# Kernel tuning notes

Measured on AMD Instinct MI355X. Metric: run time of the kernel, lower is better.

The kernel has to match this reference:

```python
import jax, jax.numpy as jnp
import numpy as np

B, N, E, K = 4, 8192, 1024, 2048  # batch, points, emb_dims, pool nodes (N//4)
KNN = 20


def _conv(w, x):  # 1x1 Conv1d, no bias: w [O,C], x [B,C,N]
    return jnp.einsum('oc,bcn->bon', w, x)


def _bn(x, s, b):  # eval-mode BN folded to per-channel scale/bias, x [B,C,N]
    return x * s[None, :, None] + b[None, :, None]


def _sqdist(a, b):  # a [B,3,N], b [B,3,M] -> [B,N,M] squared distances
    return ((a * a).sum(1)[:, :, None] + (b * b).sum(1)[:, None, :]
            - 2.0 * jnp.einsum('bcn,bcm->bnm', a, b))


def _bgather(f, idx):  # f [B,C,N], idx [B,...] -> [B,C,...]
    return jax.vmap(lambda ff, ii: ff[:, ii])(f, idx)


def _pool(xyz, feat, pw, pb, k):
    Bq, C, _ = feat.shape
    proj = _conv(pw, feat) + pb[None, :, None]          # [B,8C,N]
    vec = proj.max(-1).reshape(Bq, C, 8)                # [B,C,8]
    scores = jax.nn.sigmoid(jnp.einsum('bcn,bce->bne', feat, vec))  # [B,N,8]
    v, i = jax.lax.top_k(scores.transpose(0, 2, 1), k // 8)         # [B,8,k//8]
    values = v.transpose(0, 2, 1).reshape(Bq, -1)       # [B,k] (torch reshape order)
    idx = i.transpose(0, 2, 1).reshape(Bq, -1)
    node_static = _bgather(xyz, idx)                    # [B,3,k]
    node_feature = _bgather(feat, idx) * values[:, None, :]
    node = node_static * values[:, None, :]
    return node, node_feature, node_static


def _aggregate(xyz, node, feat, k):
    d = _sqdist(xyz, node)                               # [B,N,M]
    _, idx = jax.lax.top_k(-d.transpose(0, 2, 1), k)     # [B,M,k] nearest inputs per node
    grouped = _bgather(feat, idx)                        # [B,C,M,k]
    return grouped.max(-1)                               # [B,C,M]


def _unpool(node_xyz, unknown_xyz, feat):
    d = _sqdist(unknown_xyz, node_xyz)                   # [B,N,M]
    negd, idx = jax.lax.top_k(-d, 3)                     # 3-NN along M
    w = jax.nn.softmax(-negd, axis=-1)                   # softmax over sq-dists (faithful)
    grouped = _bgather(feat, idx)                        # [B,C,N,3]
    return (w[:, None, :, :] * grouped).sum(-1)


def _forward(x, conv1_w, bn1_s, bn1_b, conv2_w, bn2_s, bn2_b,
             conv2m_w, bn2m_s, bn2m_b, pool_w, pool_b,
             conv3_w, bn3_s, bn3_b, conv4_w, bn4_s, bn4_b,
             conv5_w, bn5_s, bn5_b, conv6_w, bn6c_s, bn6c_b,
             conv7_w, bn7c_s, bn7c_b, conv8_w, bn8_s, bn8_b,
             conv9_w, bn9_s, bn9_b, conv10_w,
             lin1_w, bn6h_s, bn6h_b, lin2_w, lin2_b, bn7h_s, bn7h_b,
             lin3_w, lin3_b):
    relu = jax.nn.relu
    xyz = x
    x1 = relu(_bn(_conv(conv1_w, x), bn1_s, bn1_b))      # [B,64,N]
    x2 = relu(_bn(_conv(conv2_w, x1), bn2_s, bn2_b))     # [B,64,N]
    xt1_ = jnp.concatenate([x1, x2], 1)                  # [B,128,N]
    xt1 = relu(_bn(_conv(conv2m_w, xt1_), bn2m_s, bn2m_b))  # [B,E,N]
    node1, nf1, node1_static = _pool(xyz, xt1_, pool_w, pool_b, K)
    agg = _aggregate(xyz, node1, xt1_, KNN)              # [B,128,K]
    h = jnp.concatenate([nf1, agg], 1)                   # [B,256,K]
    x3 = relu(_bn(_conv(conv3_w, h), bn3_s, bn3_b))
    x4 = relu(_bn(_conv(conv4_w, x3), bn4_s, bn4_b))
    xt2 = relu(_bn(_conv(conv5_w, jnp.concatenate([x3, x4], 1)), bn5_s, bn5_b))
    vector = jnp.concatenate([xt1.max(-1), xt2.max(-1)], 1)  # [B,2E]
    c = relu((vector @ lin1_w.T) * bn6h_s + bn6h_b)
    c = relu((c @ lin2_w.T + lin2_b) * bn7h_s + bn7h_b)
    logits_cls = c @ lin3_w.T + lin3_b                   # [B,15]
    vrep = jnp.broadcast_to(vector[:, :, None], (vector.shape[0], vector.shape[1], x4.shape[-1]))
    s = relu(_bn(_conv(conv6_w, jnp.concatenate([vrep, x4], 1)), bn6c_s, bn6c_b))
    s = relu(_bn(_conv(conv7_w, jnp.concatenate([s, x3], 1)), bn7c_s, bn7c_b))
    s = _unpool(node1, xyz, s)                           # [B,128,N]
    s = relu(_bn(_conv(conv8_w, jnp.concatenate([s, x2], 1)), bn8_s, bn8_b))
    s = relu(_bn(_conv(conv9_w, jnp.concatenate([s, x1], 1)), bn9_s, bn9_b))
    logits_seg = _conv(conv10_w, s)                      # [B,2,N]
    return (logits_cls, logits_seg, node1, node1_static)


def setup_inputs() -> dict:
    key = jax.random.key(0)
    keys = iter(jax.random.split(key, 80))
    def w(shape, scale=0.05):
        return jax.random.normal(next(keys), shape, jnp.float32) * scale
    inp = {'x': jax.random.normal(next(keys), (B, 3, N), jnp.float32)}
    conv_shapes = {'conv1_w': (64, 3), 'conv2_w': (64, 64), 'conv2m_w': (E, 128),
                   'conv3_w': (256, 256), 'conv4_w': (256, 256), 'conv5_w': (E, 512),
                   'conv6_w': (128, 2 * E + 256), 'conv7_w': (128, 384),
                   'conv8_w': (128, 192), 'conv9_w': (128, 192), 'conv10_w': (2, 128)}
    for n, s in conv_shapes.items():
        inp[n] = w(s)
    for n, c in [('bn1', 64), ('bn2', 64), ('bn2m', E), ('bn3', 256), ('bn4', 256),
                 ('bn5', E), ('bn6c', 128), ('bn7c', 128), ('bn8', 128), ('bn9', 128),
                 ('bn6h', 512), ('bn7h', 256)]:
        inp[n + '_s'] = 1.0 + w((c,))
        inp[n + '_b'] = w((c,))
    inp['pool_w'] = w((E, 128)); inp['pool_b'] = w((E,))
    inp['lin1_w'] = w((512, 2 * E))
    inp['lin2_w'] = w((256, 512)); inp['lin2_b'] = w((256,))
    inp['lin3_w'] = w((15, 256)); inp['lin3_b'] = w((15,))
    return inp


def reference(x, conv1_w, bn1_s, bn1_b, conv2_w, bn2_s, bn2_b,
              conv2m_w, bn2m_s, bn2m_b, pool_w, pool_b,
              conv3_w, bn3_s, bn3_b, conv4_w, bn4_s, bn4_b,
              conv5_w, bn5_s, bn5_b, conv6_w, bn6c_s, bn6c_b,
              conv7_w, bn7c_s, bn7c_b, conv8_w, bn8_s, bn8_b,
              conv9_w, bn9_s, bn9_b, conv10_w,
              lin1_w, bn6h_s, bn6h_b, lin2_w, lin2_b, bn7h_s, bn7h_b,
              lin3_w, lin3_b):
    return _forward(x, conv1_w, bn1_s, bn1_b, conv2_w, bn2_s, bn2_b,
                    conv2m_w, bn2m_s, bn2m_b, pool_w, pool_b,
                    conv3_w, bn3_s, bn3_b, conv4_w, bn4_s, bn4_b,
                    conv5_w, bn5_s, bn5_b, conv6_w, bn6c_s, bn6c_b,
                    conv7_w, bn7c_s, bn7c_b, conv8_w, bn8_s, bn8_b,
                    conv9_w, bn9_s, bn9_b, conv10_w,
                    lin1_w, bn6h_s, bn6h_b, lin2_w, lin2_b, bn7h_s, bn7h_b,
                    lin3_w, lin3_b)
```

## Files before the change

kernel.cpp:

```cpp
#include <hip/hip_runtime.h>
#include <math.h>

typedef unsigned short u16;
typedef short bf8 __attribute__((ext_vector_type(8)));
typedef float f4 __attribute__((ext_vector_type(4)));

#define NPTS 8192
#define MNODE 2048

#define WS_XT1  0L
#define WS_A    4194304L
#define WS_B    8388608L
#define WS_C    12582912L
#define WS_D    14680064L
#define WS_TOPV 18874368L
#define WS_TOPI 18882560L
#define WS_NODE 18890752L
#define WS_MAXP 18915328L
#define WS_VEC  18919424L
#define WS_C1   18927616L
#define WS_C2   18929664L
#define WS_B6   18930688L
#define WS_K20  18931200L
#define WS_K3I  19095040L
#define WS_K3W  19193344L

__device__ __forceinline__ u16 bf16rne(float f) {
    unsigned u = __float_as_uint(f);
    unsigned r = u + 0x7FFFu + ((u >> 16) & 1u);
    return (u16)(r >> 16);
}

__global__ __launch_bounds__(256) void k_conv1(const float* __restrict__ x,
                                               const float* __restrict__ W,
                                               const float* __restrict__ sc,
                                               const float* __restrict__ bi,
                                               float* __restrict__ out) {
    int t = blockIdx.x * 256 + threadIdx.x;
    int n = t & 8191, o = (t >> 13) & 63, b = t >> 19;
    const float* xb = x + (long)b * 3 * NPTS;
    float a = W[o * 3 + 0] * xb[n] + W[o * 3 + 1] * xb[NPTS + n] + W[o * 3 + 2] * xb[2 * NPTS + n];
    a = fmaxf(a * sc[o] + bi[o], 0.f);
    out[((long)b * 128 + o) * NPTS + n] = a;
}


__global__ __launch_bounds__(256) void k_packall(
        const float* __restrict__ c2mw, const float* __restrict__ c3w,
        const float* __restrict__ c4w,  const float* __restrict__ c5w,
        const float* __restrict__ c6w,  const float* __restrict__ c7w,
        const float* __restrict__ c8w,  const float* __restrict__ c9w,
        u16* __restrict__ d2m, u16* __restrict__ d3, u16* __restrict__ d4,
        u16* __restrict__ d5,  u16* __restrict__ d6, u16* __restrict__ d7,
        u16* __restrict__ d8,  u16* __restrict__ d9) {
    int t = blockIdx.x * 256 + threadIdx.x;
    const float* W; u16* dst; int C, wp, base;
    if (t < 131072)      { W = c2mw;       dst = d2m; C = 128; wp = 128;  base = 0; }
    else if (t < 196608) { W = c3w;        dst = d3;  C = 256; wp = 256;  base = 131072; }
    else if (t < 262144) { W = c4w;        dst = d4;  C = 256; wp = 256;  base = 196608; }
    else if (t < 786432) { W = c5w;        dst = d5;  C = 512; wp = 512;  base = 262144; }
    else if (t < 819200) { W = c6w + 2048; dst = d6;  C = 256; wp = 2304; base = 786432; }
    else if (t < 868352) { W = c7w;        dst = d7;  C = 384; wp = 384;  base = 819200; }
    else if (t < 892928) { W = c8w;        dst = d8;  C = 192; wp = 192;  base = 868352; }
    else if (t < 917504) { W = c9w;        dst = d9;  C = 192; wp = 192;  base = 892928; }
    else return;
    int u = t - base;
    int o = u / C, p = u - o * C;
    int blk = p >> 5, pj = p & 31;
    int g = pj >> 3, j = pj & 7;
    int k = (blk << 5) + g * 4 + (j & 3) + 16 * (j >> 2);
    dst[u] = bf16rne(W[(long)o * wp + k]);
}

__global__ __launch_bounds__(256) void k_packT2(const float* __restrict__ in, long ibs,
                                                int C, int Nn, u16* __restrict__ out,
                                                int opitch, int coff) {
    __shared__ float tile[32][33];
    int b = blockIdx.z;
    int k0 = blockIdx.y * 32, n0 = blockIdx.x * 32;
    int tx = threadIdx.x & 31, ty = threadIdx.x >> 5;
    for (int r = 0; r < 32; r += 8)
        tile[ty + r][tx] = in[(long)b * ibs + (long)(k0 + ty + r) * Nn + n0 + tx];
    __syncthreads();
    for (int r = 0; r < 32; r += 8) {
        int n = n0 + ty + r;
        int p = tx;
        int g = p >> 3, j = p & 7;
        int kin = g * 4 + (j & 3) + 16 * (j >> 2);
        out[((long)b * Nn + n) * opitch + coff + k0 + p] = bf16rne(tile[kin][ty + r]);
    }
}

__global__ __launch_bounds__(256) void k_packT2d(const float* __restrict__ in1, long ibs1, int C1,
                                                 const float* __restrict__ in2, long ibs2, int C2,
                                                 int Nn, u16* __restrict__ out, int opitch) {
    __shared__ float tile[32][33];
    int b = blockIdx.z;
    int y1 = C1 >> 5;
    const float* in; int k0, coff;
    if ((int)blockIdx.y < y1) { in = in1 + (long)b * ibs1; k0 = blockIdx.y * 32; coff = 0; }
    else { in = in2 + (long)b * ibs2; k0 = ((int)blockIdx.y - y1) * 32; coff = C1; }
    int n0 = blockIdx.x * 32;
    int tx = threadIdx.x & 31, ty = threadIdx.x >> 5;
    for (int r = 0; r < 32; r += 8)
        tile[ty + r][tx] = in[(long)(k0 + ty + r) * Nn + n0 + tx];
    __syncthreads();
    for (int r = 0; r < 32; r += 8) {
        int n = n0 + ty + r;
        int p = tx, g = p >> 3, j = p & 7;
        int kin = g * 4 + (j & 3) + 16 * (j >> 2);
        out[((long)b * Nn + n) * opitch + coff + k0 + p] = bf16rne(tile[kin][ty + r]);
    }
}

__global__ __launch_bounds__(256) void k_cvmx_bf(const u16* __restrict__ in,
                                                 const u16* __restrict__ wpk, int C,
                                                 const float* __restrict__ sc,
                                                 const float* __restrict__ bi, int do_relu,
                                                 float* __restrict__ pmax, int O, int Nn) {
    __shared__ float red[4][16][17];
    int b = blockIdx.z, nc = blockIdx.x;
    int lane = threadIdx.x & 63, w = threadIdx.x >> 6;
    int o0 = (blockIdx.y * 4 + w) * 16;
    const u16* wp = wpk + (long)(o0 + (lane & 15)) * C + ((lane >> 4) << 3);
    const u16* ip = in + ((long)b * Nn + nc * 256 + (lane & 15)) * C + ((lane >> 4) << 3);
    long nstride = 16L * C;
    f4 acc[16];
#pragma unroll
    for (int t = 0; t < 16; ++t) acc[t] = (f4)(0.f);
    for (int kk = 0; kk < C; kk += 32) {
        bf8 a = *(const bf8*)(wp + kk);
#pragma unroll
        for (int t = 0; t < 16; ++t) {
            bf8 bb = *(const bf8*)(ip + t * nstride + kk);
            acc[t] = __builtin_amdgcn_mfma_f32_16x16x32_bf16(a, bb, acc[t], 0, 0, 0);
        }
    }
#pragma unroll
    for (int j = 0; j < 4; ++j) {
        int ol = (lane >> 4) * 4 + j;
        int o = o0 + ol;
        float scv = sc ? sc[o] : 1.f;
        float biv = bi ? bi[o] : 0.f;
        float mm = -3.0e38f;
#pragma unroll
        for (int t = 0; t < 16; ++t) {
            float v = acc[t][j] * scv + biv;
            if (do_relu) v = fmaxf(v, 0.f);
            mm = fmaxf(mm, v);
        }
        red[w][ol][lane & 15] = mm;
    }
    __syncthreads();
    if (threadIdx.x < 64) {
        int ww = threadIdx.x >> 4, oo = threadIdx.x & 15;
        float mm = red[ww][oo][0];
#pragma unroll
        for (int i = 1; i < 16; ++i) mm = fmaxf(mm, red[ww][oo][i]);
        int og = (blockIdx.y * 4 + ww) * 16 + oo;
        pmax[((long)nc * 4 + b) * O + og] = mm;
    }
}

__global__ __launch_bounds__(256) void k_conv_bf(const u16* __restrict__ in,
                                                 int C,
                                                 const u16* __restrict__ wpk,
                                                 const float* __restrict__ sc,
                                                 const float* __restrict__ bi, int do_relu,
                                                 float* __restrict__ out, long obs, int Nn) {
    int b = blockIdx.z, nc = blockIdx.x;
    int lane = threadIdx.x & 63, w = threadIdx.x >> 6;
    int o0 = (blockIdx.y * 4 + w) * 16;
    const u16* wp = wpk + (long)(o0 + (lane & 15)) * C + ((lane >> 4) << 3);
    const u16* ip = in + ((long)b * Nn + nc * 256 + (lane & 15)) * C + ((lane >> 4) << 3);
    long nstride = 16L * C;
    f4 acc[16];
#pragma unroll
    for (int t = 0; t < 16; ++t) acc[t] = (f4)(0.f);
    for (int kk = 0; kk < C; kk += 32) {
        bf8 a = *(const bf8*)(wp + kk);
#pragma unroll
        for (int t = 0; t < 16; ++t) {
            bf8 bb = *(const bf8*)(ip + t * nstride + kk);
            acc[t] = __builtin_amdgcn_mfma_f32_16x16x32_bf16(a, bb, acc[t], 0, 0, 0);
        }
    }
#pragma unroll
    for (int j = 0; j < 4; ++j) {
        int o = o0 + (lane >> 4) * 4 + j;
        float scv = sc ? sc[o] : 1.f;
        float biv = bi ? bi[o] : 0.f;
        float* op = out + (long)b * obs + (long)o * Nn + nc * 256 + (lane & 15);
#pragma unroll
        for (int t = 0; t < 16; ++t) {
            float v = acc[t][j] * scv + biv;
            if (do_relu) v = fmaxf(v, 0.f);
            op[t * 16] = v;
        }
    }
}

__global__ __launch_bounds__(256) void k_conv_bf2(
        const u16* __restrict__ in1, int p1, int C1,
        const u16* __restrict__ in2, int p2, int C2,
        const u16* __restrict__ wpk,
        const float* __restrict__ extra,
        const float* __restrict__ sc, const float* __restrict__ bi, int do_relu,
        float* __restrict__ out, long obs, int O, int Nn) {
    int b = blockIdx.z, nc = blockIdx.x;
    int lane = threadIdx.x & 63, w = threadIdx.x >> 6;
    int o0 = (blockIdx.y * 4 + w) * 16;
    int Ct = C1 + C2;
    const u16* wp = wpk + (long)(o0 + (lane & 15)) * Ct + ((lane >> 4) << 3);
    f4 acc[16];
#pragma unroll
    for (int t = 0; t < 16; ++t) acc[t] = (f4)(0.f);
    {
        const u16* ip1 = in1 + ((long)b * Nn + nc * 256 + (lane & 15)) * p1 + ((lane >> 4) << 3);
        long ns1 = 16L * p1;
        for (int kk = 0; kk < C1; kk += 32) {
            bf8 a = *(const bf8*)(wp + kk);
#pragma unroll
            for (int t = 0; t < 16; ++t) {
                bf8 bb = *(const bf8*)(ip1 + t * ns1 + kk);
                acc[t] = __builtin_amdgcn_mfma_f32_16x16x32_bf16(a, bb, acc[t], 0, 0, 0);
            }
        }
    }
    if (in2) {
        const u16* ip2 = in2 + ((long)b * Nn + nc * 256 + (lane & 15)) * p2 + ((lane >> 4) << 3);
        long ns2 = 16L * p2;
        for (int kk = 0; kk < C2; kk += 32) {
            bf8 a = *(const bf8*)(wp + C1 + kk);
#pragma unroll
            for (int t = 0; t < 16; ++t) {
                bf8 bb = *(const bf8*)(ip2 + t * ns2 + kk);
                acc[t] = __builtin_amdgcn_mfma_f32_16x16x32_bf16(a, bb, acc[t], 0, 0, 0);
            }
        }
    }
#pragma unroll
    for (int j = 0; j < 4; ++j) {
        int o = o0 + (lane >> 4) * 4 + j;
        float e = extra ? extra[(long)b * O + o] : 0.f;
        float scv = sc ? sc[o] : 1.f;
        float biv = bi ? bi[o] : 0.f;
        float* op = out + (long)b * obs + (long)o * Nn + nc * 256 + (lane & 15);
#pragma unroll
        for (int t = 0; t < 16; ++t) {
            float v = (acc[t][j] + e) * scv + biv;
            if (do_relu) v = fmaxf(v, 0.f);
            op[t * 16] = v;
        }
    }
}

#define CMAX_FMA16()                                                        \
    {                                                                       \
        const float4* wp4 = reinterpret_cast<const float4*>(Wl + c16);      \
        _Pragma("unroll")                                                   \
        for (int g = 0; g < 4; ++g) {                                       \
            float4 w = wp4[g];                                              \
            acc[4 * g + 0].x = fmaf(w.x, v.x, acc[4 * g + 0].x);            \
            acc[4 * g + 0].y = fmaf(w.x, v.y, acc[4 * g + 0].y);            \
            acc[4 * g + 0].z = fmaf(w.x, v.z, acc[4 * g + 0].z);            \
            acc[4 * g + 0].w = fmaf(w.x, v.w, acc[4 * g + 0].w);            \
            acc[4 * g + 1].x = fmaf(w.y, v.x, acc[4 * g + 1].x);            \
            acc[4 * g + 1].y = fmaf(w.y, v.y, acc[4 * g + 1].y);            \
            acc[4 * g + 1].z = fmaf(w.y, v.z, acc[4 * g + 1].z);            \
            acc[4 * g + 1].w = fmaf(w.y, v.w, acc[4 * g + 1].w);            \
            acc[4 * g + 2].x = fmaf(w.z, v.x, acc[4 * g + 2].x);            \
            acc[4 * g + 2].y = fmaf(w.z, v.y, acc[4 * g + 2].y);            \
            acc[4 * g + 2].z = fmaf(w.z, v.z, acc[4 * g + 2].z);            \
            acc[4 * g + 2].w = fmaf(w.z, v.w, acc[4 * g + 2].w);            \
            acc[4 * g + 3].x = fmaf(w.w, v.x, acc[4 * g + 3].x);            \
            acc[4 * g + 3].y = fmaf(w.w, v.y, acc[4 * g + 3].y);            \
            acc[4 * g + 3].z = fmaf(w.w, v.z, acc[4 * g + 3].z);            \
            acc[4 * g + 3].w = fmaf(w.w, v.w, acc[4 * g + 3].w);            \
        }                                                                   \
    }

__global__ __launch_bounds__(256) void k_convmax(
        const float* __restrict__ in, int C, long ibs,
        const float* __restrict__ W1, const float* __restrict__ cb1,
        const float* __restrict__ sc1, const float* __restrict__ bi1, int relu1,
        float* __restrict__ pmax1,
        const float* __restrict__ W2, const float* __restrict__ cb2,
        const float* __restrict__ sc2, const float* __restrict__ bi2, int relu2,
        float* __restrict__ pmax2,
        int wpitch, int O, int Nn) {
    extern __shared__ float sm_[];
    float* Wl = sm_;
    float* red = sm_;
    int b = blockIdx.z;
    int ns = blockIdx.x;
    int oblocks = O >> 4;
    int setid = (int)blockIdx.y / oblocks;
    int og0 = ((int)blockIdx.y - setid * oblocks) * 16;
    const float* W  = setid ? W2 : W1;
    const float* cb = setid ? cb2 : cb1;
    const float* sc = setid ? sc2 : sc1;
    const float* bi = setid ? bi2 : bi1;
    int do_relu     = setid ? relu2 : relu1;
    float* pmax     = setid ? pmax2 : pmax1;
    for (int t = threadIdx.x; t < 16 * C; t += 256) {
        int c = t >> 4, o = t & 15;
        Wl[t] = W[(long)(og0 + o) * wpitch + c];
    }
    __syncthreads();
    int n0 = ns * 1024 + threadIdx.x * 4;
    float4 acc[16];
#pragma unroll
    for (int o = 0; o < 16; ++o) acc[o] = make_float4(0.f, 0.f, 0.f, 0.f);
    const float* p = in + (long)b * ibs + n0;
    float4 v = *reinterpret_cast<const float4*>(p);
    for (int c = 0; c < C - 1; ++c) {
        float4 vn = *reinterpret_cast<const float4*>(p + (long)(c + 1) * Nn);
        int c16 = c * 16;
        CMAX_FMA16();
        v = vn;
    }
    {
        int c16 = (C - 1) * 16;
        CMAX_FMA16();
    }
    float h2[16];
#pragma unroll
    for (int o = 0; o < 16; ++o) {
        float cbv = cb ? cb[og0 + o] : 0.f;
        float scv = sc ? sc[og0 + o] : 1.f;
        float biv = bi ? bi[og0 + o] : 0.f;
        float4 a = acc[o];
        float vx = (a.x + cbv) * scv + biv;
        float vy = (a.y + cbv) * scv + biv;
        float vz = (a.z + cbv) * scv + biv;
        float vw = (a.w + cbv) * scv + biv;
        if (do_relu) {
            vx = fmaxf(vx, 0.f); vy = fmaxf(vy, 0.f);
            vz = fmaxf(vz, 0.f); vw = fmaxf(vw, 0.f);
        }
        h2[o] = fmaxf(fmaxf(vx, vy), fmaxf(vz, vw));
    }
    __syncthreads();
#pragma unroll
    for (int o = 0; o < 16; ++o) red[o * 257 + threadIdx.x] = h2[o];
    __syncthreads();
    for (int ls = 7; ls >= 0; --ls) {
        int s = 1 << ls;
        for (int w = threadIdx.x; w < 16 * s; w += 256) {
            int o = w >> ls, i = w & (s - 1);
            float* r = red + o * 257;
            r[i] = fmaxf(r[i], r[i + s]);
        }
        __syncthreads();
    }
    if (threadIdx.x < 16)
        pmax[((long)ns * 4 + b) * O + og0 + threadIdx.x] = red[threadIdx.x * 257];
}

__global__ __launch_bounds__(256) void k_maxred2(const float* __restrict__ pA, int nsA, int OA,
                                                 float* __restrict__ outA, long obsA,
                                                 const float* __restrict__ pB, int nsB, int OB,
                                                 float* __restrict__ outB, long obsB,
                                                 int blocksA) {
    const float* pm; int ns, O; float* out; long obs; int bid = blockIdx.x;
    if (bid < blocksA) { pm = pA; ns = nsA; O = OA; out = outA; obs = obsA; }
    else { pm = pB; ns = nsB; O = OB; out = outB; obs = obsB; bid -= blocksA; }
    int t = bid * 256 + threadIdx.x;
    if (t >= 4 * O) return;
    int o = t % O, b = t / O;
    float m = -3.0e38f;
    for (int s = 0; s < ns; ++s) m = fmaxf(m, pm[((long)s * 4 + b) * O + o]);
    out[(long)b * obs + o] = m;
}

__global__ __launch_bounds__(256) void k_maxred(const float* __restrict__ pmax, int nsplit,
                                                int O, float* __restrict__ out, long obs) {
    int t = blockIdx.x * 256 + threadIdx.x;
    if (t >= 4 * O) return;
    int o = t % O, b = t / O;
    float m = -3.0e38f;
    for (int s = 0; s < nsplit; ++s) m = fmaxf(m, pmax[((long)s * 4 + b) * O + o]);
    out[(long)b * obs + o] = m;
}

#define CONV_FMA8()                                                         \
    {                                                                       \
        const float4* wp4 = reinterpret_cast<const float4*>(Wl + c8);       \
        _Pragma("unroll")                                                   \
        for (int g = 0; g < 2; ++g) {                                       \
            float4 w = wp4[g];                                              \
            acc[4 * g + 0].x = fmaf(w.x, v.x, acc[4 * g + 0].x);            \
            acc[4 * g + 0].y = fmaf(w.x, v.y, acc[4 * g + 0].y);            \
            acc[4 * g + 0].z = fmaf(w.x, v.z, acc[4 * g + 0].z);            \
            acc[4 * g + 0].w = fmaf(w.x, v.w, acc[4 * g + 0].w);            \
            acc[4 * g + 1].x = fmaf(w.y, v.x, acc[4 * g + 1].x);            \
            acc[4 * g + 1].y = fmaf(w.y, v.y, acc[4 * g + 1].y);            \
            acc[4 * g + 1].z = fmaf(w.y, v.z, acc[4 * g + 1].z);            \
            acc[4 * g + 1].w = fmaf(w.y, v.w, acc[4 * g + 1].w);            \
            acc[4 * g + 2].x = fmaf(w.z, v.x, acc[4 * g + 2].x);            \
            acc[4 * g + 2].y = fmaf(w.z, v.y, acc[4 * g + 2].y);            \
            acc[4 * g + 2].z = fmaf(w.z, v.z, acc[4 * g + 2].z);            \
            acc[4 * g + 2].w = fmaf(w.z, v.w, acc[4 * g + 2].w);            \
            acc[4 * g + 3].x = fmaf(w.w, v.x, acc[4 * g + 3].x);            \
            acc[4 * g + 3].y = fmaf(w.w, v.y, acc[4 * g + 3].y);            \
            acc[4 * g + 3].z = fmaf(w.w, v.z, acc[4 * g + 3].z);            \
            acc[4 * g + 3].w = fmaf(w.w, v.w, acc[4 * g + 3].w);            \
        }                                                                   \
    }

__global__ __launch_bounds__(256) void k_conv(const float* __restrict__ in1, int C1, long ibs1,
                                              const float* __restrict__ in2, int C2, long ibs2,
                                              const float* __restrict__ W, int wpitch,
                                              const float* __restrict__ extra,
                                              const float* __restrict__ sc,
                                              const float* __restrict__ bi, int do_relu,
                                              float* __restrict__ out, long obs, int O, int Nn) {
    __shared__ float Wl[384 * 8];
    int b = blockIdx.z;
    int og0 = blockIdx.y * 8;
    int on = O - og0; if (on > 8) on = 8;
    int Ct = C1 + C2;
    for (int t = threadIdx.x; t < Ct * 8; t += 256) {
        int c = t >> 3, o = t & 7;
        Wl[t] = (o < on) ? W[(long)(og0 + o) * wpitch + c] : 0.f;
    }
    __syncthreads();
    int n0 = blockIdx.x * 1024 + threadIdx.x * 4;
    float4 acc[8];
#pragma unroll
    for (int o = 0; o < 8; ++o) acc[o] = make_float4(0.f, 0.f, 0.f, 0.f);
    const float* p1 = in1 + (long)b * ibs1 + n0;
    {
        float4 v = *reinterpret_cast<const float4*>(p1);
        for (int c = 0; c < C1 - 1; ++c) {
            float4 vn = *reinterpret_cast<const float4*>(p1 + (long)(c + 1) * Nn);
            int c8 = c * 8;
            CONV_FMA8();
            v = vn;
        }
        int c8 = (C1 - 1) * 8;
        CONV_FMA8();
    }
    if (in2) {
        const float* p2 = in2 + (long)b * ibs2 + n0;
        float4 v = *reinterpret_cast<const float4*>(p2);
        for (int c = 0; c < C2 - 1; ++c) {
            float4 vn = *reinterpret_cast<const float4*>(p2 + (long)(c + 1) * Nn);
            int c8 = (C1 + c) * 8;
            CONV_FMA8();
            v = vn;
        }
        int c8 = (Ct - 1) * 8;
        CONV_FMA8();
    }
#pragma unroll
    for (int o = 0; o < 8; ++o) {
        if (o < on) {
            float e = extra ? extra[(long)b * O + og0 + o] : 0.f;
            float s = sc ? sc[og0 + o] : 1.f;
            float bv = bi ? bi[og0 + o] : 0.f;
            float4 a = acc[o];
            a.x = (a.x + e) * s + bv;
            a.y = (a.y + e) * s + bv;
            a.z = (a.z + e) * s + bv;
            a.w = (a.w + e) * s + bv;
            if (do_relu) {
                a.x = fmaxf(a.x, 0.f); a.y = fmaxf(a.y, 0.f);
                a.z = fmaxf(a.z, 0.f); a.w = fmaxf(a.w, 0.f);
            }
            *reinterpret_cast<float4*>(out + (long)b * obs + (long)(og0 + o) * Nn + n0) = a;
        }
    }
}

__global__ __launch_bounds__(256) void k_scores(const float* __restrict__ feat,
                                                const float* __restrict__ maxp,
                                                float* __restrict__ scores) {
    __shared__ float vl[1024];
    int b = blockIdx.z;
    for (int t = threadIdx.x; t < 1024; t += 256) vl[t] = maxp[b * 1024 + t];
    __syncthreads();
    int n = blockIdx.x * 256 + threadIdx.x;
    float acc[8];
#pragma unroll
    for (int e = 0; e < 8; ++e) acc[e] = 0.f;
    const float* p = feat + (long)b * 128 * NPTS + n;
    float v = p[0];
    for (int c = 0; c < 127; ++c) {
        float vn = p[(long)(c + 1) * NPTS];
#pragma unroll
        for (int e = 0; e < 8; ++e) acc[e] = fmaf(vl[c * 8 + e], v, acc[e]);
        v = vn;
    }
#pragma unroll
    for (int e = 0; e < 8; ++e) acc[e] = fmaf(vl[127 * 8 + e], v, acc[e]);
#pragma unroll
    for (int e = 0; e < 8; ++e)
        scores[((long)b * 8 + e) * NPTS + n] = 1.f / (1.f + expf(-acc[e]));
}

__global__ __launch_bounds__(256) void k_sorta(const float* __restrict__ scores,
                                               unsigned int* __restrict__ kout,
                                               unsigned short* __restrict__ iout) {
    __shared__ unsigned int kv[1024];
    __shared__ unsigned short ki[1024];
    int ch = blockIdx.x & 7;
    const float* sp = scores + (long)(blockIdx.x >> 3) * NPTS + ch * 1024;
    for (int t = threadIdx.x; t < 1024; t += 256) {
        kv[t] = __float_as_uint(sp[t]) ^ 0xFFFFFFFFu;
        ki[t] = (unsigned short)(ch * 1024 + t);
    }
    __syncthreads();
    for (int k = 2; k <= 1024; k <<= 1) {
        for (int j = k >> 1; j > 0; j >>= 1) {
            for (int t = threadIdx.x; t < 1024; t += 256) {
                int ixj = t ^ j;
                if (ixj > t) {
                    unsigned int va = kv[t], vb = kv[ixj];
                    unsigned short ia = ki[t], ib = ki[ixj];
                    bool up = ((t & k) == 0);
                    bool gt = (va > vb) || (va == vb && ia > ib);
                    if (gt == up) { kv[t] = vb; kv[ixj] = va; ki[t] = ib; ki[ixj] = ia; }
                }
            }
            __syncthreads();
        }
    }
    if (threadIdx.x < 256) {
        kout[blockIdx.x * 256 + threadIdx.x] = kv[threadIdx.x];
        iout[blockIdx.x * 256 + threadIdx.x] = ki[threadIdx.x];
    }
}

__global__ __launch_bounds__(512) void k_sortb(const unsigned int* __restrict__ kin,
                                               const unsigned short* __restrict__ iin,
                                               float* __restrict__ topv,
                                               int* __restrict__ topi) {
    __shared__ unsigned int kv[2048];
    __shared__ unsigned short ki[2048];
    int be = blockIdx.x, b = be >> 3, e = be & 7;
    for (int t = threadIdx.x; t < 2048; t += 512) {
        kv[t] = kin[be * 2048 + t];
        ki[t] = iin[be * 2048 + t];
    }
    __syncthreads();
    for (int k = 2; k <= 2048; k <<= 1) {
        for (int j = k >> 1; j > 0; j >>= 1) {
            for (int t = threadIdx.x; t < 2048; t += 512) {
                int ixj = t ^ j;
                if (ixj > t) {
                    unsigned int va = kv[t], vb = kv[ixj];
                    unsigned short ia = ki[t], ib = ki[ixj];
                    bool up = ((t & k) == 0);
                    bool gt = (va > vb) || (va == vb && ia > ib);
                    if (gt == up) { kv[t] = vb; kv[ixj] = va; ki[t] = ib; ki[ixj] = ia; }
                }
            }
            __syncthreads();
        }
    }
    for (int r = threadIdx.x; r < 256; r += 512) {
        int j = r * 8 + e;
        topv[b * 2048 + j] = __uint_as_float(kv[r] ^ 0xFFFFFFFFu);
        topi[b * 2048 + j] = (int)ki[r];
    }
}

__global__ __launch_bounds__(256) void k_gather(const float* __restrict__ feat,
                                                const float* __restrict__ xyz,
                                                const float* __restrict__ topv,
                                                const int* __restrict__ topi,
                                                float* __restrict__ h,
                                                float* __restrict__ node_ws,
                                                float* __restrict__ out_node,
                                                float* __restrict__ out_nstat) {
    int bid = blockIdx.x;
    if (bid < 4096) {
        int t = bid * 256 + threadIdx.x;
        int j = t & 2047, c = (t >> 11) & 127, b = t >> 18;
        int i = topi[b * 2048 + j];
        float v = topv[b * 2048 + j];
        h[((long)b * 256 + c) * MNODE + j] = feat[((long)b * 128 + c) * NPTS + i] * v;
    } else {
        int t = (bid - 4096) * 256 + threadIdx.x;
        int j = t & 2047, b = t >> 11;
        int i = topi[b * 2048 + j];
        float v = topv[b * 2048 + j];
#pragma unroll
        for (int k = 0; k < 3; ++k) {
            float sx = xyz[((long)b * 3 + k) * NPTS + i];
            float nd = sx * v;
            out_nstat[((long)b * 3 + k) * MNODE + j] = sx;
            out_node[((long)b * 3 + k) * MNODE + j] = nd;
            node_ws[((long)b * 3 + k) * MNODE + j] = nd;
        }
    }
}

__device__ __forceinline__ unsigned int fsortbits(float f) {
    unsigned int u = __float_as_uint(f);
    return u ^ ((unsigned int)((int)u >> 31) | 0x80000000u);
}

__global__ __launch_bounds__(256) void k_knn20(const float* __restrict__ xyz,
                                               const float* __restrict__ node,
                                               int* __restrict__ k20) {
    __shared__ unsigned int s1[256];
    __shared__ int s2[256];
    __shared__ int lcnt;
    int m = blockIdx.x & 2047, b = blockIdx.x >> 11;
    int t = threadIdx.x;
    float nx = node[((long)b * 3 + 0) * MNODE + m];
    float ny = node[((long)b * 3 + 1) * MNODE + m];
    float nz = node[((long)b * 3 + 2) * MNODE + m];
    float sm = nx * nx + ny * ny + nz * nz;
    const float* xb = xyz + (long)b * 3 * NPTS;
    unsigned int kmin = 0xFFFFFFFFu;
    for (int i = 0; i < 32; ++i) {
        int n = i * 256 + t;
        float px = xb[n], py = xb[NPTS + n], pz = xb[2 * NPTS + n];
        float d = (px * px + py * py + pz * pz) + sm - 2.f * (px * nx + py * ny + pz * nz);
        unsigned int key = fsortbits(d);
        kmin = key < kmin ? key : kmin;
    }
    s1[t] = kmin;
    if (t == 0) lcnt = 0;
    __syncthreads();
    for (int k = 2; k <= 256; k <<= 1) {
        for (int j = k >> 1; j > 0; j >>= 1) {
            int ixj = t ^ j;
            if (ixj > t) {
                unsigned int va = s1[t], vb = s1[ixj];
                bool up = ((t & k) == 0);
                if ((va > vb) == up) { s1[t] = vb; s1[ixj] = va; }
            }
            __syncthreads();
        }
    }
    unsigned int keyT = s1[19];
    __syncthreads();
    for (int i = 0; i < 32; ++i) {
        int n = i * 256 + t;
        float px = xb[n], py = xb[NPTS + n], pz = xb[2 * NPTS + n];
        float d = (px * px + py * py + pz * pz) + sm - 2.f * (px * nx + py * ny + pz * nz);
        unsigned int key = fsortbits(d);
        if (key <= keyT) {
            int p = atomicAdd(&lcnt, 1);
            if (p < 128) { s1[p] = key; s2[p] = n; }
        }
    }
    __syncthreads();
    int cnt = lcnt;
    if (cnt <= 128) {
        if (t >= cnt && t < 128) { s1[t] = 0xFFFFFFFFu; s2[t] = 0x7FFFFFFF; }
        __syncthreads();
        for (int k = 2; k <= 128; k <<= 1) {
            for (int j = k >> 1; j > 0; j >>= 1) {
                if (t < 128) {
                    int ixj = t ^ j;
                    if (ixj > t) {
                        unsigned int va = s1[t], vb = s1[ixj];
                        int ia = s2[t], ib = s2[ixj];
                        bool up = ((t & k) == 0);
                        bool gt = (va > vb) || (va == vb && ia > ib);
                        if (gt == up) { s1[t] = vb; s1[ixj] = va; s2[t] = ib; s2[ixj] = ia; }
                    }
                }
                __syncthreads();
            }
        }
        if (t < 20) k20[((long)b * 2048 + m) * 20 + t] = s2[t];
    } else {
        unsigned int lastk = 0u; int lasti = -1;
        for (int r = 0; r < 20; ++r) {
            unsigned int bk = 0xFFFFFFFFu; int bi = 0x7FFFFFFF;
            for (int i = 0; i < 32; ++i) {
                int n = i * 256 + t;
                float px = xb[n], py = xb[NPTS + n], pz = xb[2 * NPTS + n];
                float d = (px * px + py * py + pz * pz) + sm - 2.f * (px * nx + py * ny + pz * nz);
                unsigned int key = fsortbits(d);
                bool gtlast = (key > lastk) || (key == lastk && n > lasti);
                bool ltbest = (key < bk) || (key == bk && n < bi);
                if (gtlast && ltbest) { bk = key; bi = n; }
            }
            s1[t] = bk; s2[t] = bi;
            __syncthreads();
            for (int s = 128; s > 0; s >>= 1) {
                if (t < s) {
                    unsigned int vo = s1[t + s]; int io = s2[t + s];
                    unsigned int vm = s1[t]; int im = s2[t];
                    if (vo < vm || (vo == vm && io < im)) { s1[t] = vo; s2[t] = io; }
                }
                __syncthreads();
            }
            if (t == 0) k20[((long)b * 2048 + m) * 20 + r] = s2[0];
            lastk = s1[0]; lasti = s2[0];
            __syncthreads();
        }
    }
}

__global__ __launch_bounds__(256) void k_agg(const float* __restrict__ feat,
                                             const int* __restrict__ k20,
                                             float* __restrict__ h) {
    int t = blockIdx.x * 256 + threadIdx.x;
    int m = t & 2047, c = (t >> 11) & 127, b = t >> 18;
    const int* ip = k20 + ((long)b * 2048 + m) * 20;
    const float* fb = feat + ((long)b * 128 + c) * NPTS;
    float mx = -3.0e38f;
#pragma unroll
    for (int q = 0; q < 20; ++q) mx = fmaxf(mx, fb[ip[q] & 8191]);
    h[((long)b * 256 + 128 + c) * MNODE + m] = mx;
}

__global__ __launch_bounds__(256) void k_gemv(const float* __restrict__ in, int C,
                                              const float* __restrict__ W, int wpitch,
                                              const float* __restrict__ lb,
                                              const float* __restrict__ sc,
                                              const float* __restrict__ bi, int do_relu,
                                              float* __restrict__ out, int O) {
    __shared__ float red[256];
    int o = blockIdx.x;
    int t = threadIdx.x;
    const float* wp = W + (long)o * wpitch;
    float a0 = 0.f, a1 = 0.f, a2 = 0.f, a3 = 0.f;
    for (int c = t * 4; c < C; c += 1024) {
        float4 w = *reinterpret_cast<const float4*>(wp + c);
        float4 v0 = *reinterpret_cast<const float4*>(in + 0L * C + c);
        float4 v1 = *reinterpret_cast<const float4*>(in + 1L * C + c);
        float4 v2 = *reinterpret_cast<const float4*>(in + 2L * C + c);
        float4 v3 = *reinterpret_cast<const float4*>(in + 3L * C + c);
        a0 += w.x * v0.x + w.y * v0.y + w.z * v0.z + w.w * v0.w;
        a1 += w.x * v1.x + w.y * v1.y + w.z * v1.z + w.w * v1.w;
        a2 += w.x * v2.x + w.y * v2.y + w.z * v2.z + w.w * v2.w;
        a3 += w.x * v3.x + w.y * v3.y + w.z * v3.z + w.w * v3.w;
    }
    float lbv = lb ? lb[o] : 0.f;
    float scv = sc ? sc[o] : 1.f;
    float biv = bi ? bi[o] : 0.f;
#pragma unroll
    for (int b = 0; b < 4; ++b) {
        float a = (b == 0) ? a0 : (b == 1) ? a1 : (b == 2) ? a2 : a3;
        __syncthreads();
        red[t] = a;
        __syncthreads();
        for (int s2 = 128; s2 > 0; s2 >>= 1) {
            if (t < s2) red[t] += red[t + s2];
            __syncthreads();
        }
        if (t == 0) {
            float r = (red[0] + lbv) * scv + biv;
            if (do_relu) r = fmaxf(r, 0.f);
            out[(long)b * O + o] = r;
        }
    }
}

__global__ __launch_bounds__(256) void k_knn3(const float* __restrict__ xyz,
                                              const float* __restrict__ node,
                                              int* __restrict__ k3i, float* __restrict__ k3w) {
    __shared__ float sx[2048], sy[2048], sz[2048], sn[2048];
    __shared__ float md[256][3];
    __shared__ int   mi[256][3];
    int b = blockIdx.x >> 8;
    int pbase = (blockIdx.x & 255) * 32;
    int t = threadIdx.x;
    const float* nb = node + (long)b * 3 * MNODE;
    for (int j = t; j < 2048; j += 256) {
        float qx = nb[j], qy = nb[MNODE + j], qz = nb[2 * MNODE + j];
        sx[j] = qx; sy[j] = qy; sz[j] = qz;
        sn[j] = qx * qx + qy * qy + qz * qz;
    }
    __syncthreads();
    int i = t & 31, q = t >> 5;
    int n = pbase + i;
    float px = xyz[((long)b * 3 + 0) * NPTS + n];
    float py = xyz[((long)b * 3 + 1) * NPTS + n];
    float pz = xyz[((long)b * 3 + 2) * NPTS + n];
    float sp = px * px + py * py + pz * pz;
    float d0 = 3.0e38f, d1 = 3.0e38f, d2 = 3.0e38f;
    int i0 = 0, i1 = 0, i2 = 0;
    int m0 = q * 256;
#pragma unroll 4
    for (int k = 0; k < 256; ++k) {
        int m = m0 + k;
        float d = (sp + sn[m]) - 2.f * (px * sx[m] + py * sy[m] + pz * sz[m]);
        if (d < d2) {
            d2 = d; i2 = m;
            if (d2 < d1) { float td = d1; d1 = d2; d2 = td; int ti = i1; i1 = i2; i2 = ti; }
            if (d1 < d0) { float td = d0; d0 = d1; d1 = td; int ti = i0; i0 = i1; i1 = ti; }
        }
    }
    md[t][0] = d0; md[t][1] = d1; md[t][2] = d2;
    mi[t][0] = i0; mi[t][1] = i1; mi[t][2] = i2;
    __syncthreads();
    if (t < 32) {
        int p0 = 0, p1 = 0, p2 = 0, p3 = 0, p4 = 0, p5 = 0, p6 = 0, p7 = 0;
        float rd[3]; int ri[3];
#pragma unroll
        for (int r = 0; r < 3; ++r) {
            float bestd = 3.0e38f; int besti = 0x7FFFFFFF; int bestq = -1;
#define KNN3_HEAD(QQ, PV)                                                              \
            {                                                                          \
                float dd = md[(QQ) * 32 + t][PV]; int ii = mi[(QQ) * 32 + t][PV];      \
                if (dd < bestd || (dd == bestd && ii < besti)) {                       \
                    bestd = dd; besti = ii; bestq = (QQ);                              \
                }                                                                      \
            }
            KNN3_HEAD(0, p0) KNN3_HEAD(1, p1) KNN3_HEAD(2, p2) KNN3_HEAD(3, p3)
            KNN3_HEAD(4, p4) KNN3_HEAD(5, p5) KNN3_HEAD(6, p6) KNN3_HEAD(7, p7)
#undef KNN3_HEAD
            rd[r] = bestd; ri[r] = besti;
            p0 += (bestq == 0); p1 += (bestq == 1); p2 += (bestq == 2); p3 += (bestq == 3);
            p4 += (bestq == 4); p5 += (bestq == 5); p6 += (bestq == 6); p7 += (bestq == 7);
        }
        float mxd = fmaxf(rd[0], fmaxf(rd[1], rd[2]));
        float e0 = expf(rd[0] - mxd), e1 = expf(rd[1] - mxd), e2 = expf(rd[2] - mxd);
        float inv = 1.f / (e0 + e1 + e2);
        long base = ((long)b * NPTS + pbase + t) * 3;
        k3i[base] = ri[0]; k3i[base + 1] = ri[1]; k3i[base + 2] = ri[2];
        k3w[base] = e0 * inv; k3w[base + 1] = e1 * inv; k3w[base + 2] = e2 * inv;
    }
}

__global__ __launch_bounds__(256) void k_unpool(const float* __restrict__ s7,
                                                const int* __restrict__ k3i,
                                                const float* __restrict__ k3w,
                                                float* __restrict__ sup) {
    int t = blockIdx.x * 256 + threadIdx.x;
    int n = t & 8191, c = (t >> 13) & 127, b = t >> 20;
    long base = ((long)b * NPTS + n) * 3;
    const float* spp = s7 + ((long)b * 128 + c) * MNODE;
    float a = k3w[base] * spp[k3i[base]] + k3w[base + 1] * spp[k3i[base + 1]] +
              k3w[base + 2] * spp[k3i[base + 2]];
    sup[((long)b * 128 + c) * NPTS + n] = a;
}

extern "C" void kernel_launch(void* const* d_in, const int* in_sizes, int n_in,
                              void* d_out, int out_size, void* d_ws, size_t ws_size,
                              hipStream_t stream) {
    const float* x     = (const float*)d_in[0];
    const float* c1w   = (const float*)d_in[1];
    const float* c2w   = (const float*)d_in[2];
    const float* c2mw  = (const float*)d_in[3];
    const float* c3w   = (const float*)d_in[4];
    const float* c4w   = (const float*)d_in[5];
    const float* c5w   = (const float*)d_in[6];
    const float* c6w   = (const float*)d_in[7];
    const float* c7w   = (const float*)d_in[8];
    const float* c8w   = (const float*)d_in[9];
    const float* c9w   = (const float*)d_in[10];
    const float* c10w  = (const float*)d_in[11];
    const float* bn1s  = (const float*)d_in[12]; const float* bn1b  = (const float*)d_in[13];
    const float* bn2s  = (const float*)d_in[14]; const float* bn2b  = (const float*)d_in[15];
    const float* bn2ms = (const float*)d_in[16]; const float* bn2mb = (const float*)d_in[17];
    const float* bn3s  = (const float*)d_in[18]; const float* bn3b  = (const float*)d_in[19];
    const float* bn4s  = (const float*)d_in[20]; const float* bn4b  = (const float*)d_in[21];
    const float* bn5s  = (const float*)d_in[22]; const float* bn5b  = (const float*)d_in[23];
    const float* bn6cs = (const float*)d_in[24]; const float* bn6cb = (const float*)d_in[25];
    const float* bn7cs = (const float*)d_in[26]; const float* bn7cb = (const float*)d_in[27];
    const float* bn8s  = (const float*)d_in[28]; const float* bn8b  = (const float*)d_in[29];
    const float* bn9s  = (const float*)d_in[30]; const float* bn9b  = (const float*)d_in[31];
    const float* bn6hs = (const float*)d_in[32]; const float* bn6hb = (const float*)d_in[33];
    const float* bn7hs = (const float*)d_in[34]; const float* bn7hb = (const float*)d_in[35];
    const float* poolw = (const float*)d_in[36]; const float* poolb = (const float*)d_in[37];
    const float* l1w   = (const float*)d_in[38];
    const float* l2w   = (const float*)d_in[39]; const float* l2b   = (const float*)d_in[40];
    const float* l3w   = (const float*)d_in[41]; const float* l3b   = (const float*)d_in[42];

    float* ws   = (float*)d_ws;
    float* xt1  = ws + WS_XT1;
    float* x34  = ws + WS_A;
    float* s8   = ws + WS_A;
    float* scor = ws + WS_B;
    float* hbuf = ws + WS_C;
    float* s6   = ws + WS_C;
    float* s7   = ws + WS_C + 1048576L;
    float* sup  = ws + WS_D;
    float* s9   = ws + WS_D;
    float* topv = ws + WS_TOPV;
    int*   topi = (int*)(ws + WS_TOPI);
    float* node = ws + WS_NODE;
    float* maxp = ws + WS_MAXP;
    float* vec  = ws + WS_VEC;
    float* c1b  = ws + WS_C1;
    float* c2b_ = ws + WS_C2;
    float* b6   = ws + WS_B6;
    int*   k20  = (int*)(ws + WS_K20);
    float* pmax1 = ws + WS_K20;
    float* pmax2 = ws + WS_K20 + 131072;
    int*   k3i  = (int*)(ws + WS_K3I);
    float* k3w  = ws + WS_K3W;
    unsigned int*   sskeys = (unsigned int*)(ws + WS_A);
    unsigned short* ssidx  = (unsigned short*)(ws + WS_A + 65536);
    u16* xtb   = (u16*)(ws + WS_C);
    u16* c2mwb = (u16*)(ws + WS_D);
    u16* x34b  = (u16*)(ws + WS_B);
    u16* c5wb  = (u16*)(ws + WS_B + 2097152);
    u16* hb    = (u16*)(ws + WS_D);
    u16* x3p   = (u16*)(ws + WS_D + 1048576);
    u16* c3wb  = (u16*)(ws + WS_D + 2097152);
    u16* c4wb  = (u16*)(ws + WS_D + 2129920);
    u16* c6wb  = (u16*)(ws + WS_D + 2162688);
    u16* c7wb  = (u16*)(ws + WS_D + 2179072);
    u16* s6p   = (u16*)(ws + WS_D);
    u16* sp8   = (u16*)(ws + WS_B);
    u16* cc8wb = (u16*)(ws + WS_B + 3145728);
    u16* cc9wb = (u16*)(ws + WS_B + 3158016);
    u16* sp9   = (u16*)(ws + WS_B);

    float* out       = (float*)d_out;
    float* out_cls   = out;
    float* out_seg   = out + 60;
    float* out_node  = out + 60 + 65536;
    float* out_nstat = out_node + 24576;

    k_packall<<<dim3(3584), dim3(256), 0, stream>>>(c2mw, c3w, c4w, c5w, c6w, c7w, c8w, c9w,
                                                    c2mwb, c3wb, c4wb, c5wb, c6wb, c7wb,
                                                    cc8wb, cc9wb);
    k_conv1<<<dim3(8192), dim3(256), 0, stream>>>(x, c1w, bn1s, bn1b, xt1);
    k_conv<<<dim3(8, 8, 4), dim3(256), 0, stream>>>(xt1, 64, 128L * NPTS, nullptr, 0, 0,
                                                    c2w, 64, nullptr, bn2s, bn2b, 1,
                                                    xt1 + 64L * NPTS, 128L * NPTS, 64, NPTS);
    k_packT2<<<dim3(256, 4, 4), dim3(256), 0, stream>>>(xt1, 128L * NPTS, 128, NPTS, xtb, 128, 0);
    k_cvmx_bf<<<dim3(32, 16, 4), dim3(256), 0, stream>>>(xtb, c2mwb, 128,
                                                         bn2ms, bn2mb, 1, pmax1, 1024, NPTS);
    k_convmax<<<dim3(8, 64, 4), dim3(256), 16 * 257 * 4, stream>>>(
        xt1, 128, 128L * NPTS,
        poolw, poolb, nullptr, nullptr, 0, pmax2,
        nullptr, nullptr, nullptr, nullptr, 0, nullptr,
        128, 1024, NPTS);
    k_maxred2<<<dim3(32), dim3(256), 0, stream>>>(pmax1, 32, 1024, vec, 2048,
                                                  pmax2, 8, 1024, maxp, 1024, 16);
    k_scores<<<dim3(32, 1, 4), dim3(256), 0, stream>>>(xt1, maxp, scor);
    k_sorta<<<dim3(256), dim3(256), 0, stream>>>(scor, sskeys, ssidx);
    k_sortb<<<dim3(32), dim3(512), 0, stream>>>(sskeys, ssidx, topv, topi);
    k_gather<<<dim3(4128), dim3(256), 0, stream>>>(xt1, x, topv, topi, hbuf,
                                                   node, out_node, out_nstat);
    k_knn20<<<dim3(8192), dim3(256), 0, stream>>>(x, node, k20);
    k_agg<<<dim3(4096), dim3(256), 0, stream>>>(xt1, k20, hbuf);
    k_packT2<<<dim3(64, 8, 4), dim3(256), 0, stream>>>(hbuf, 256L * MNODE, 256, MNODE, hb, 256, 0);
    k_conv_bf<<<dim3(8, 4, 4), dim3(256), 0, stream>>>(hb, 256, c3wb, bn3s, bn3b, 1,
                                                       x34, 512L * MNODE, MNODE);
    k_packT2<<<dim3(64, 8, 4), dim3(256), 0, stream>>>(x34, 512L * MNODE, 256, MNODE, x3p, 256, 0);
    k_conv_bf<<<dim3(8, 4, 4), dim3(256), 0, stream>>>(x3p, 256, c4wb, bn4s, bn4b, 1,
                                                       x34 + 256L * MNODE, 512L * MNODE, MNODE);
    k_packT2<<<dim3(64, 16, 4), dim3(256), 0, stream>>>(x34, 512L * MNODE, 512, MNODE, x34b, 512, 0);
    k_cvmx_bf<<<dim3(8, 16, 4), dim3(256), 0, stream>>>(x34b, c5wb, 512,
                                                        bn5s, bn5b, 1, pmax1, 1024, MNODE);
    k_maxred<<<dim3(16), dim3(256), 0, stream>>>(pmax1, 8, 1024, vec + 1024, 2048);
    k_gemv<<<dim3(512), dim3(256), 0, stream>>>(vec, 2048, l1w, 2048, nullptr, bn6hs, bn6hb, 1, c1b, 512);
    k_gemv<<<dim3(256), dim3(256), 0, stream>>>(c1b, 512, l2w, 512, l2b, bn7hs, bn7hb, 1, c2b_, 256);
    k_gemv<<<dim3(15), dim3(256), 0, stream>>>(c2b_, 256, l3w, 256, l3b, nullptr, nullptr, 0, out_cls, 15);
    k_gemv<<<dim3(128), dim3(256), 0, stream>>>(vec, 2048, c6w, 2304, nullptr, nullptr, nullptr, 0, b6, 128);
    k_conv_bf2<<<dim3(8, 2, 4), dim3(256), 0, stream>>>(x34b + 256, 512, 256,
                                                        nullptr, 0, 0, c6wb, b6,
                                                        bn6cs, bn6cb, 1,
                                                        s6, 128L * MNODE, 128, MNODE);
    k_packT2<<<dim3(64, 4, 4), dim3(256), 0, stream>>>(s6, 128L * MNODE, 128, MNODE, s6p, 128, 0);
    k_conv_bf2<<<dim3(8, 2, 4), dim3(256), 0, stream>>>(s6p, 128, 128,
                                                        x34b, 512, 256, c7wb, nullptr,
                                                        bn7cs, bn7cb, 1,
                                                        s7, 128L * MNODE, 128, MNODE);
    k_knn3<<<dim3(1024), dim3(256), 0, stream>>>(x, node, k3i, k3w);
    k_unpool<<<dim3(16384), dim3(256), 0, stream>>>(s7, k3i, k3w, sup);
    k_packT2d<<<dim3(256, 6, 4), dim3(256), 0, stream>>>(sup, 128L * NPTS, 128,
                                                         xt1 + 64L * NPTS, 128L * NPTS, 64,
                                                         NPTS, sp8, 192);
    k_conv_bf<<<dim3(32, 2, 4), dim3(256), 0, stream>>>(sp8, 192, cc8wb, bn8s, bn8b, 1,
                                                        s8, 128L * NPTS, NPTS);
    k_packT2d<<<dim3(256, 6, 4), dim3(256), 0, stream>>>(s8, 128L * NPTS, 128,
                                                         xt1, 128L * NPTS, 64,
                                                         NPTS, sp9, 192);
    k_conv_bf<<<dim3(32, 2, 4), dim3(256), 0, stream>>>(sp9, 192, cc9wb, bn9s, bn9b, 1,
                                                        s9, 128L * NPTS, NPTS);
    k_conv<<<dim3(8, 1, 4), dim3(256), 0, stream>>>(s9, 128, 128L * NPTS, nullptr, 0, 0,
                                                    c10w, 128, nullptr, nullptr, nullptr, 0,
                                                    out_seg, 2L * NPTS, 2, NPTS);
    (void)in_sizes; (void)n_in; (void)out_size; (void)ws_size;
}
```

Baseline: 806.4 us.

## Fuse bf16 packing into conv epilogues to drop separate transpose-pack passes

Adds a conv kernel variant whose epilogue writes bf16 directly into the packed point-major layout (with the MFMA k-permutation) expected by the next conv. Conv3, conv4, conv6 and conv8 now use it, which removes several fp32 intermediate writes and their k_packT2/k_packT2d repack launches. The xt1 slice for the conv9 input is packed up front into a relocated buffer. The cost is strided scattered 2-byte stores in the epilogue instead of coalesced fp32 stores.

```diff
diff --git a/kernel.cpp b/kernel.cpp
--- a/kernel.cpp
+++ b/kernel.cpp
@@ -29,6 +29,11 @@
     unsigned u = __float_as_uint(f);
     unsigned r = u + 0x7FFFu + ((u >> 16) & 1u);
     return (u16)(r >> 16);
+}
+
+__device__ __forceinline__ int packpos(int o) {
+    int k = o & 31;
+    return (o & ~31) + ((k & 15) >> 2) * 8 + (k >> 4) * 4 + (k & 3);
 }
 
 __global__ __launch_bounds__(256) void k_conv1(const float* __restrict__ x,
@@ -196,6 +201,46 @@
             float v = acc[t][j] * scv + biv;
             if (do_relu) v = fmaxf(v, 0.f);
             op[t * 16] = v;
+        }
+    }
+}
+
+__global__ __launch_bounds__(256) void k_conv_bfp(
+        const u16* __restrict__ in1, int p1, int C1,
+        const u16* __restrict__ wpk,
+        const float* __restrict__ extra,
+        const float* __restrict__ sc, const float* __restrict__ bi, int do_relu,
+        u16* __restrict__ outp, int opitch, int ocoff, int O, int Nn) {
+    int b = blockIdx.z, nc = blockIdx.x;
+    int lane = threadIdx.x & 63, w = threadIdx.x >> 6;
+    int o0 = (blockIdx.y * 4 + w) * 16;
+    const u16* wp = wpk + (long)(o0 + (lane & 15)) * C1 + ((lane >> 4) << 3);
+    const u16* ip = in1 + ((long)b * Nn + nc * 256 + (lane & 15)) * p1 + ((lane >> 4) << 3);
+    long nstride = 16L * p1;
+    f4 acc[16];
+#pragma unroll
+    for (int t = 0; t < 16; ++t) acc[t] = (f4)(0.f);
+    for (int kk = 0; kk < C1; kk += 32) {
+        bf8 a = *(const bf8*)(wp + kk);
+#pragma unroll
+        for (int t = 0; t < 16; ++t) {
+            bf8 bb = *(const bf8*)(ip + t * nstride + kk);
+            acc[t] = __builtin_amdgcn_mfma_f32_16x16x32_bf16(a, bb, acc[t], 0, 0, 0);
+        }
+    }
+    int nbase = nc * 256 + (lane & 15);
+#pragma unroll
+    for (int j = 0; j < 4; ++j) {
+        int o = o0 + (lane >> 4) * 4 + j;
+        float e = extra ? extra[(long)b * O + o] : 0.f;
+        float scv = sc ? sc[o] : 1.f;
+        float biv = bi ? bi[o] : 0.f;
+        int pp = ocoff + packpos(o);
+#pragma unroll
+        for (int t = 0; t < 16; ++t) {
+            float v = (acc[t][j] + e) * scv + biv;
+            if (do_relu) v = fmaxf(v, 0.f);
+            outp[((long)b * Nn + nbase + t * 16) * opitch + pp] = bf16rne(v);
         }
     }
 }
@@ -871,11 +916,8 @@
 
     float* ws   = (float*)d_ws;
     float* xt1  = ws + WS_XT1;
-    float* x34  = ws + WS_A;
-    float* s8   = ws + WS_A;
     float* scor = ws + WS_B;
     float* hbuf = ws + WS_C;
-    float* s6   = ws + WS_C;
     float* s7   = ws + WS_C + 1048576L;
     float* sup  = ws + WS_D;
     float* s9   = ws + WS_D;
@@ -899,7 +941,6 @@
     u16* x34b  = (u16*)(ws + WS_B);
     u16* c5wb  = (u16*)(ws + WS_B + 2097152);
     u16* hb    = (u16*)(ws + WS_D);
-    u16* x3p   = (u16*)(ws + WS_D + 1048576);
     u16* c3wb  = (u16*)(ws + WS_D + 2097152);
     u16* c4wb  = (u16*)(ws + WS_D + 2129920);
     u16* c6wb  = (u16*)(ws + WS_D + 2162688);
@@ -908,7 +949,7 @@
     u16* sp8   = (u16*)(ws + WS_B);
     u16* cc8wb = (u16*)(ws + WS_B + 3145728);
     u16* cc9wb = (u16*)(ws + WS_B + 3158016);
-    u16* sp9   = (u16*)(ws + WS_B);
+    u16* sp9   = (u16*)(ws + WS_A);
 
     float* out       = (float*)d_out;
     float* out_cls   = out;
@@ -941,12 +982,10 @@
     k_knn20<<<dim3(8192), dim3(256), 0, stream>>>(x, node, k20);
     k_agg<<<dim3(4096), dim3(256), 0, stream>>>(xt1, k20, hbuf);
     k_packT2<<<dim3(64, 8, 4), dim3(256), 0, stream>>>(hbuf, 256L * MNODE, 256, MNODE, hb, 256, 0);
-    k_conv_bf<<<dim3(8, 4, 4), dim3(256), 0, stream>>>(hb, 256, c3wb, bn3s, bn3b, 1,
-                                                       x34, 512L * MNODE, MNODE);
-    k_packT2<<<dim3(64, 8, 4), dim3(256), 0, stream>>>(x34, 512L * MNODE, 256, MNODE, x3p, 256, 0);
-    k_conv_bf<<<dim3(8, 4, 4), dim3(256), 0, stream>>>(x3p, 256, c4wb, bn4s, bn4b, 1,
-                                                       x34 + 256L * MNODE, 512L * MNODE, MNODE);
-    k_packT2<<<dim3(64, 16, 4), dim3(256), 0, stream>>>(x34, 512L * MNODE, 512, MNODE, x34b, 512, 0);
+    k_conv_bfp<<<dim3(8, 4, 4), dim3(256), 0, stream>>>(hb, 256, 256, c3wb, nullptr,
+                                                        bn3s, bn3b, 1, x34b, 512, 0, 256, MNODE);
+    k_conv_bfp<<<dim3(8, 4, 4), dim3(256), 0, stream>>>(x34b, 512, 256, c4wb, nullptr,
+                                                        bn4s, bn4b, 1, x34b, 512, 256, 256, MNODE);
     k_cvmx_bf<<<dim3(8, 16, 4), dim3(256), 0, stream>>>(x34b, c5wb, 512,
                                                         bn5s, bn5b, 1, pmax1, 1024, MNODE);
     k_maxred<<<dim3(16), dim3(256), 0, stream>>>(pmax1, 8, 1024, vec + 1024, 2048);
@@ -954,25 +993,20 @@
     k_gemv<<<dim3(256), dim3(256), 0, stream>>>(c1b, 512, l2w, 512, l2b, bn7hs, bn7hb, 1, c2b_, 256);
     k_gemv<<<dim3(15), dim3(256), 0, stream>>>(c2b_, 256, l3w, 256, l3b, nullptr, nullptr, 0, out_cls, 15);
     k_gemv<<<dim3(128), dim3(256), 0, stream>>>(vec, 2048, c6w, 2304, nullptr, nullptr, nullptr, 0, b6, 128);
-    k_conv_bf2<<<dim3(8, 2, 4), dim3(256), 0, stream>>>(x34b + 256, 512, 256,
-                                                        nullptr, 0, 0, c6wb, b6,
-                                                        bn6cs, bn6cb, 1,
-                                                        s6, 128L * MNODE, 128, MNODE);
-    k_packT2<<<dim3(64, 4, 4), dim3(256), 0, stream>>>(s6, 128L * MNODE, 128, MNODE, s6p, 128, 0);
+    k_conv_bfp<<<dim3(8, 2, 4), dim3(256), 0, stream>>>(x34b + 256, 512, 256, c6wb, b6,
+                                                        bn6cs, bn6cb, 1, s6p, 128, 0, 128, MNODE);
     k_conv_bf2<<<dim3(8, 2, 4), dim3(256), 0, stream>>>(s6p, 128, 128,
                                                         x34b, 512, 256, c7wb, nullptr,
                                                         bn7cs, bn7cb, 1,
                                                         s7, 128L * MNODE, 128, MNODE);
     k_knn3<<<dim3(1024), dim3(256), 0, stream>>>(x, node, k3i, k3w);
     k_unpool<<<dim3(16384), dim3(256), 0, stream>>>(s7, k3i, k3w, sup);
+    k_packT2<<<dim3(256, 2, 4), dim3(256), 0, stream>>>(xt1, 128L * NPTS, 64, NPTS, sp9, 192, 128);
     k_packT2d<<<dim3(256, 6, 4), dim3(256), 0, stream>>>(sup, 128L * NPTS, 128,
                                                          xt1 + 64L * NPTS, 128L * NPTS, 64,
                                                          NPTS, sp8, 192);
-    k_conv_bf<<<dim3(32, 2, 4), dim3(256), 0, stream>>>(sp8, 192, cc8wb, bn8s, bn8b, 1,
-                                                        s8, 128L * NPTS, NPTS);
-    k_packT2d<<<dim3(256, 6, 4), dim3(256), 0, stream>>>(s8, 128L * NPTS, 128,
-                                                         xt1, 128L * NPTS, 64,
-                                                         NPTS, sp9, 192);
+    k_conv_bfp<<<dim3(32, 2, 4), dim3(256), 0, stream>>>(sp8, 192, 192, cc8wb, nullptr,
+                                                         bn8s, bn8b, 1, sp9, 192, 0, 128, NPTS);
     k_conv_bf<<<dim3(32, 2, 4), dim3(256), 0, stream>>>(sp9, 192, cc9wb, bn9s, bn9b, 1,
                                                         s9, 128L * NPTS, NPTS);
     k_conv<<<dim3(8, 1, 4), dim3(256), 0, stream>>>(s9, 128, 128L * NPTS, nullptr, 0, 0,
```

Result: no change. 813.1 us (+0.8%).
